# Optimization experiments

Hardware: AMD Instinct MI355X
Metric: run time of the kernel (lower is better)

## Reference

```python
import jax, jax.numpy as jnp
import numpy as np

NUM_LOOP = 10


def gru_cell(x, h, W_ih, W_hh, b_ih, b_hh):
    # torch.nn.GRUCell math. x, h: [N, H]; W_ih, W_hh: [3H, H]; b: [3H]
    gi = x @ W_ih.T + b_ih
    gh = h @ W_hh.T + b_hh
    i_r, i_z, i_n = jnp.split(gi, 3, axis=-1)
    h_r, h_z, h_n = jnp.split(gh, 3, axis=-1)
    r = jax.nn.sigmoid(i_r + h_r)
    z = jax.nn.sigmoid(i_z + h_z)
    n = jnp.tanh(i_n + r * h_n)
    return (1.0 - z) * n + z * h


def setup_inputs() -> dict:
    key = jax.random.key(0)
    ks = jax.random.split(key, 16)
    B, S, L, H, V = 16, 128, 128, 128, 50000
    input_var = jax.random.randint(ks[0], (B, S, L), 0, V, dtype=jnp.int32)
    adjacency = (jax.random.uniform(ks[1], (B, S, L, L)) < 0.05).astype(jnp.float32)
    u = lambda k, shp, a: jax.random.uniform(k, shp, minval=-a, maxval=a, dtype=jnp.float32)
    emb = jax.random.normal(ks[2], (V, H), dtype=jnp.float32) * 0.1
    gnn_w = u(ks[3], (H, H), 0.08)
    gnn_b = u(ks[4], (H,), 0.08)
    W_ih = u(ks[5], (3 * H, H), 0.08)
    W_hh = u(ks[6], (3 * H, H), 0.08)
    b_ih = u(ks[7], (3 * H,), 0.08)
    b_hh = u(ks[8], (3 * H,), 0.08)
    mW1 = u(ks[9], (H, H), 0.08)
    mb1 = u(ks[10], (H,), 0.08)
    mW2 = u(ks[11], (H, H), 0.08)
    mb2 = u(ks[12], (H,), 0.08)
    mW3 = u(ks[13], (1, H), 0.08)
    mb3 = u(ks[14], (1,), 0.08)
    return dict(input_var=input_var, adjacency=adjacency, emb=emb, gnn_w=gnn_w,
                gnn_b=gnn_b, W_ih=W_ih, W_hh=W_hh, b_ih=b_ih, b_hh=b_hh,
                mW1=mW1, mb1=mb1, mW2=mW2, mb2=mb2, mW3=mW3, mb3=mb3)


def reference(input_var, adjacency, emb, gnn_w, gnn_b, W_ih, W_hh, b_ih, b_hh,
              mW1, mb1, mW2, mb2, mW3, mb3):
    B, S, L = input_var.shape
    H = emb.shape[1]
    node_feature = emb[input_var]  # [B, S, L, H]

    def body(i, nf):
        tmp = nf @ gnn_w + gnn_b                      # [B,S,L,H] linear transform
        agg = jnp.matmul(adjacency, tmp)              # [B,S,L,L] @ [B,S,L,H]
        h = gru_cell(agg.reshape(-1, H), nf.reshape(-1, H), W_ih, W_hh, b_ih, b_hh)
        return h.reshape(B, S, L, H)

    node_feature = jax.lax.fori_loop(0, NUM_LOOP, body, node_feature)
    x = node_feature.reshape(B, S * L, H)
    # mention_predictor: 3-layer MLP with tanh after every layer (incl. last)
    h1 = jnp.tanh(x @ mW1.T + mb1)
    h2 = jnp.tanh(h1 @ mW2.T + mb2)
    mention_score = jnp.tanh(h2 @ mW3.T + mb3)        # [B, S*L, 1]
    return mention_score.reshape(B, S * L)
```

## Files before the change

kernel.cpp:

```cpp
#include <hip/hip_runtime.h>
#include <stdint.h>

typedef __bf16 bf16x8 __attribute__((ext_vector_type(8)));
typedef float  f32x4  __attribute__((ext_vector_type(4)));
typedef unsigned short ushortx4 __attribute__((ext_vector_type(4)));

#define LDS_NFROW 0
#define LDS_NFT   32768
#define LDS_P     65536
#define LDS_SAT   98304
#define LDS_RSA   131072
#define LDS_GB2   131584
#define LDS_BIH   133120
#define LDS_BHH   134656
#define LDS_MB1   136192
#define LDS_MB2   136704
#define LDS_TOTAL 137216

#define WS_GW2T   0
#define WS_WHH    98304
#define WS_MW1    196608
#define WS_MW2    229376
#define WS_GB2    262144

__device__ __forceinline__ unsigned short f2bf(float f){
  union{float f; uint32_t u;} v; v.f = f;
  return (unsigned short)((v.u + 0x7FFFu + ((v.u>>16)&1u)) >> 16);
}
__device__ __forceinline__ float bf2f(unsigned short h){
  union{uint32_t u; float f;} v; v.u = ((uint32_t)h)<<16; return v.f;
}
__device__ __forceinline__ float fast_sigmoid(float x){
  float t = __builtin_amdgcn_exp2f(-1.442695041f*x);
  return __builtin_amdgcn_rcpf(1.0f + t);
}
__device__ __forceinline__ float fast_tanh(float x){
  float t = __builtin_amdgcn_exp2f(-2.885390082f*x);
  return 2.0f*__builtin_amdgcn_rcpf(1.0f + t) - 1.0f;
}
__device__ __forceinline__ uint32_t sw(uint32_t row, uint32_t col){
  return row*256u + ((((col>>3) ^ (row&7)) << 4) | ((col&7)<<1));
}

extern "C" __global__ __launch_bounds__(128) void gnn_prep(
    const float* __restrict__ Wih, const float* __restrict__ Whh,
    const float* __restrict__ gnnw, const float* __restrict__ gnnb,
    const float* __restrict__ mW1, const float* __restrict__ mW2,
    unsigned short* __restrict__ gw2t, unsigned short* __restrict__ whhb,
    unsigned short* __restrict__ mw1b, unsigned short* __restrict__ mw2b,
    float* __restrict__ gb2)
{
  __shared__ float wg[128];
  const int b = blockIdx.x, t = threadIdx.x;
  if (b < 384){
    wg[t] = Wih[b*128 + t];
    __syncthreads();
    float acc = 0.f;
    for (int h=0; h<128; ++h) acc += wg[h] * gnnw[t*128 + h];
    gw2t[b*128 + t] = f2bf(acc);
    if (t == 0){
      float a2 = 0.f;
      for (int h=0; h<128; ++h) a2 += wg[h] * gnnb[h];
      gb2[b] = a2;
    }
  } else if (b < 416){
    int base = (b-384)*1536;
    for (int i=t; i<1536; i+=128) whhb[base+i] = f2bf(Whh[base+i]);
  } else if (b < 432){
    int base = (b-416)*1024;
    for (int i=t; i<1024; i+=128) mw1b[base+i] = f2bf(mW1[base+i]);
  } else if (b < 448){
    int base = (b-432)*1024;
    for (int i=t; i<1024; i+=128) mw2b[base+i] = f2bf(mW2[base+i]);
  }
}

extern "C" __global__ __launch_bounds__(512) void gnn_main(
    const int* __restrict__ iv, const float* __restrict__ adj,
    const float* __restrict__ emb,
    const float* __restrict__ bih, const float* __restrict__ bhh,
    const float* __restrict__ mb1, const float* __restrict__ mb2,
    const float* __restrict__ mW3, const float* __restrict__ mb3,
    const __bf16* __restrict__ gw2t, const __bf16* __restrict__ whhb,
    const __bf16* __restrict__ mw1b, const __bf16* __restrict__ mw2b,
    const float* __restrict__ gb2, float* __restrict__ out)
{
  extern __shared__ char lds[];
  const int bs   = blockIdx.x;
  const int tid  = threadIdx.x;
  const int w    = tid >> 6;
  const int lane = tid & 63;
  const int n16  = lane & 15;
  const int q    = lane >> 4;
  const f32x4 zf4 = {0.f, 0.f, 0.f, 0.f};

  if (tid < 384){
    *(float*)(lds + LDS_GB2 + tid*4) = gb2[tid];
    *(float*)(lds + LDS_BIH + tid*4) = bih[tid];
    *(float*)(lds + LDS_BHH + tid*4) = bhh[tid];
  }
  if (tid >= 384){
    int t = tid - 384;
    *(float*)(lds + LDS_MB1 + t*4) = mb1[t];
    *(float*)(lds + LDS_MB2 + t*4) = mb2[t];
  }

  {
    const int l  = tid >> 2;
    const int hc = (tid & 3) * 32;
    const int row = iv[bs*128 + l];
    const float* src = emb + (size_t)row*128 + hc;
    #pragma unroll
    for (int c=0; c<4; ++c){
      float4 f0 = *(const float4*)(src + c*8);
      float4 f1 = *(const float4*)(src + c*8 + 4);
      union{ bf16x8 v; unsigned short s8[8]; } u;
      u.s8[0]=f2bf(f0.x); u.s8[1]=f2bf(f0.y); u.s8[2]=f2bf(f0.z); u.s8[3]=f2bf(f0.w);
      u.s8[4]=f2bf(f1.x); u.s8[5]=f2bf(f1.y); u.s8[6]=f2bf(f1.z); u.s8[7]=f2bf(f1.w);
      *(bf16x8*)(lds + LDS_NFROW + sw(l, hc + c*8)) = u.v;
      #pragma unroll
      for (int j=0; j<8; ++j)
        *(unsigned short*)(lds + LDS_NFT + sw(hc + c*8 + j, l)) = u.s8[j];
    }
  }

  {
    const float* abase = adj + (size_t)bs * 16384;
    #pragma unroll
    for (int k=0; k<4; ++k){
      int s   = k*512 + tid;
      int sl  = s & 63;
      int chk = s >> 6;
      int ltg = chk >> 2, ks = chk & 3;
      int al  = ltg*16 + (sl & 15);
      int ak  = ks*32 + (sl >> 4) * 8;
      const float* p = abase + al*128 + ak;
      float4 f0 = *(const float4*)(p);
      float4 f1 = *(const float4*)(p + 4);
      union{ bf16x8 v; unsigned short s8[8]; } u;
      u.s8[0]=f2bf(f0.x); u.s8[1]=f2bf(f0.y); u.s8[2]=f2bf(f0.z); u.s8[3]=f2bf(f0.w);
      u.s8[4]=f2bf(f1.x); u.s8[5]=f2bf(f1.y); u.s8[6]=f2bf(f1.z); u.s8[7]=f2bf(f1.w);
      *(bf16x8*)(lds + LDS_SAT + s*16) = u.v;
    }
    int l = tid >> 2, p4 = tid & 3;
    const float* p = abase + l*128 + p4*32;
    float ssum = 0.f;
    #pragma unroll
    for (int c=0; c<8; ++c){
      float4 f = *(const float4*)(p + c*4);
      ssum += f.x + f.y + f.z + f.w;
    }
    ssum += __shfl_xor(ssum, 1);
    ssum += __shfl_xor(ssum, 2);
    if (p4 == 0) *(float*)(lds + LDS_RSA + l*4) = ssum;
  }
  __syncthreads();

  const int wr = w & 1, wc = w >> 1;
  const int t0 = wr*64, l0 = wc*32;
  const int h0 = w*16;

  const __bf16* gAr = gw2t + (size_t)(h0       + n16) * 128;
  const __bf16* gAz = gw2t + (size_t)(h0 + 128 + n16) * 128;
  const __bf16* gAn = gw2t + (size_t)(h0 + 256 + n16) * 128;
  const __bf16* hAr = whhb + (size_t)(h0       + n16) * 128;
  const __bf16* hAz = whhb + (size_t)(h0 + 128 + n16) * 128;
  const __bf16* hAn = whhb + (size_t)(h0 + 256 + n16) * 128;

  for (int it=0; it<10; ++it){
    f32x4 accA[4][2];
    #pragma unroll
    for (int a=0; a<4; ++a){ accA[a][0] = zf4; accA[a][1] = zf4; }
    for (int ks=0; ks<4; ++ks){
      bf16x8 af[4];
      #pragma unroll
      for (int tt=0; tt<4; ++tt)
        af[tt] = *(const bf16x8*)(lds + LDS_NFT + sw(t0 + tt*16 + n16, ks*32 + q*8));
      #pragma unroll
      for (int lb=0; lb<2; ++lb){
        int chunk = (wc*2 + lb)*4 + ks;
        bf16x8 bfb = *(const bf16x8*)(lds + LDS_SAT + (chunk*64 + lane)*16);
        #pragma unroll
        for (int tt=0; tt<4; ++tt)
          accA[tt][lb] = __builtin_amdgcn_mfma_f32_16x16x32_bf16(af[tt], bfb, accA[tt][lb], 0,0,0);
      }
    }
    #pragma unroll
    for (int tt=0; tt<4; ++tt){
      #pragma unroll
      for (int lb=0; lb<2; ++lb){
        int l  = l0 + lb*16 + n16;
        int tb = t0 + tt*16 + q*4;
        ushortx4 o4;
        #pragma unroll
        for (int r=0; r<4; ++r) o4[r] = f2bf(accA[tt][lb][r]);
        *(ushortx4*)(lds + LDS_P + sw(l, tb)) = o4;
      }
    }
    __syncthreads();

    f32x4 aR[8], aZ[8], aGN[8], aHN[8];
    #pragma unroll
    for (int i=0; i<8; ++i){ aR[i]=zf4; aZ[i]=zf4; aGN[i]=zf4; aHN[i]=zf4; }
    for (int ks=0; ks<4; ++ks){
      int koff = ks*32 + q*8;
      bf16x8 f_gr = *(const bf16x8*)(gAr + koff);
      bf16x8 f_gz = *(const bf16x8*)(gAz + koff);
      bf16x8 f_gn = *(const bf16x8*)(gAn + koff);
      bf16x8 f_hr = *(const bf16x8*)(hAr + koff);
      bf16x8 f_hz = *(const bf16x8*)(hAz + koff);
      bf16x8 f_hn = *(const bf16x8*)(hAn + koff);
      #pragma unroll
      for (int lt=0; lt<8; ++lt){
        int l = lt*16 + n16;
        bf16x8 bp = *(const bf16x8*)(lds + LDS_P     + sw(l, koff));
        bf16x8 bh = *(const bf16x8*)(lds + LDS_NFROW + sw(l, koff));
        aR[lt]  = __builtin_amdgcn_mfma_f32_16x16x32_bf16(f_gr, bp, aR[lt], 0,0,0);
        aR[lt]  = __builtin_amdgcn_mfma_f32_16x16x32_bf16(f_hr, bh, aR[lt], 0,0,0);
        aZ[lt]  = __builtin_amdgcn_mfma_f32_16x16x32_bf16(f_gz, bp, aZ[lt], 0,0,0);
        aZ[lt]  = __builtin_amdgcn_mfma_f32_16x16x32_bf16(f_hz, bh, aZ[lt], 0,0,0);
        aGN[lt] = __builtin_amdgcn_mfma_f32_16x16x32_bf16(f_gn, bp, aGN[lt], 0,0,0);
        aHN[lt] = __builtin_amdgcn_mfma_f32_16x16x32_bf16(f_hn, bh, aHN[lt], 0,0,0);
      }
    }
    __syncthreads();

    float c_gr[4], c_gz[4], c_gn[4], c_br[4], c_bz[4], c_bin[4], c_bhn[4];
    #pragma unroll
    for (int r=0; r<4; ++r){
      int h = h0 + q*4 + r;
      c_gr[r]  = *(const float*)(lds + LDS_GB2 + h*4);
      c_gz[r]  = *(const float*)(lds + LDS_GB2 + (128+h)*4);
      c_gn[r]  = *(const float*)(lds + LDS_GB2 + (256+h)*4);
      c_br[r]  = *(const float*)(lds + LDS_BIH + h*4)       + *(const float*)(lds + LDS_BHH + h*4);
      c_bz[r]  = *(const float*)(lds + LDS_BIH + (128+h)*4) + *(const float*)(lds + LDS_BHH + (128+h)*4);
      c_bin[r] = *(const float*)(lds + LDS_BIH + (256+h)*4);
      c_bhn[r] = *(const float*)(lds + LDS_BHH + (256+h)*4);
    }
    #pragma unroll
    for (int lt=0; lt<8; ++lt){
      int l = lt*16 + n16;
      float rs = *(const float*)(lds + LDS_RSA + l*4);
      uint32_t a_nf = sw(l, h0 + q*4);
      ushortx4 old4 = *(const ushortx4*)(lds + LDS_NFROW + a_nf);
      ushortx4 new4;
      #pragma unroll
      for (int r=0; r<4; ++r){
        float xr = aR[lt][r] + rs*c_gr[r] + c_br[r];
        float xz = aZ[lt][r] + rs*c_gz[r] + c_bz[r];
        float rg = fast_sigmoid(xr);
        float zg = fast_sigmoid(xz);
        float xn = (aGN[lt][r] + rs*c_gn[r] + c_bin[r]) + rg*(aHN[lt][r] + c_bhn[r]);
        float ng = fast_tanh(xn);
        float hv = bf2f(old4[r]);
        new4[r] = f2bf(ng + zg*(hv - ng));
      }
      *(ushortx4*)(lds + LDS_NFROW + a_nf) = new4;
      #pragma unroll
      for (int r=0; r<4; ++r)
        *(unsigned short*)(lds + LDS_NFT + sw(h0 + q*4 + r, l)) = new4[r];
    }
    __syncthreads();
  }

  {
    f32x4 acc[4][2];
    #pragma unroll
    for (int a=0; a<4; ++a){ acc[a][0] = zf4; acc[a][1] = zf4; }
    for (int ks=0; ks<4; ++ks){
      int koff = ks*32 + q*8;
      bf16x8 af[4];
      #pragma unroll
      for (int tt=0; tt<4; ++tt)
        af[tt] = *(const bf16x8*)(mw1b + (size_t)(t0 + tt*16 + n16)*128 + koff);
      #pragma unroll
      for (int lb=0; lb<2; ++lb){
        int l = l0 + lb*16 + n16;
        bf16x8 bb = *(const bf16x8*)(lds + LDS_NFROW + sw(l, koff));
        #pragma unroll
        for (int tt=0; tt<4; ++tt)
          acc[tt][lb] = __builtin_amdgcn_mfma_f32_16x16x32_bf16(af[tt], bb, acc[tt][lb], 0,0,0);
      }
    }
    #pragma unroll
    for (int tt=0; tt<4; ++tt){
      #pragma unroll
      for (int lb=0; lb<2; ++lb){
        int l  = l0 + lb*16 + n16;
        int ob = t0 + tt*16 + q*4;
        ushortx4 o4;
        #pragma unroll
        for (int r=0; r<4; ++r){
          float bsv = *(const float*)(lds + LDS_MB1 + (ob + r)*4);
          o4[r] = f2bf(fast_tanh(acc[tt][lb][r] + bsv));
        }
        *(ushortx4*)(lds + LDS_P + sw(l, ob)) = o4;
      }
    }
  }
  __syncthreads();

  {
    f32x4 acc[4][2];
    #pragma unroll
    for (int a=0; a<4; ++a){ acc[a][0] = zf4; acc[a][1] = zf4; }
    for (int ks=0; ks<4; ++ks){
      int koff = ks*32 + q*8;
      bf16x8 af[4];
      #pragma unroll
      for (int tt=0; tt<4; ++tt)
        af[tt] = *(const bf16x8*)(mw2b + (size_t)(t0 + tt*16 + n16)*128 + koff);
      #pragma unroll
      for (int lb=0; lb<2; ++lb){
        int l = l0 + lb*16 + n16;
        bf16x8 bb = *(const bf16x8*)(lds + LDS_P + sw(l, koff));
        #pragma unroll
        for (int tt=0; tt<4; ++tt)
          acc[tt][lb] = __builtin_amdgcn_mfma_f32_16x16x32_bf16(af[tt], bb, acc[tt][lb], 0,0,0);
      }
    }
    #pragma unroll
    for (int tt=0; tt<4; ++tt){
      #pragma unroll
      for (int lb=0; lb<2; ++lb){
        int l  = l0 + lb*16 + n16;
        int ob = t0 + tt*16 + q*4;
        ushortx4 o4;
        #pragma unroll
        for (int r=0; r<4; ++r){
          float bsv = *(const float*)(lds + LDS_MB2 + (ob + r)*4);
          o4[r] = f2bf(fast_tanh(acc[tt][lb][r] + bsv));
        }
        *(ushortx4*)(lds + LDS_NFT + sw(l, ob)) = o4;
      }
    }
  }
  __syncthreads();

  {
    int l = tid >> 2, p4 = tid & 3;
    float dot = 0.f;
    #pragma unroll
    for (int c=0; c<4; ++c){
      int o = p4*32 + c*8;
      union{ bf16x8 v; unsigned short s8[8]; } u;
      u.v = *(const bf16x8*)(lds + LDS_NFT + sw(l, o));
      float4 w0 = *(const float4*)(mW3 + o);
      float4 w1 = *(const float4*)(mW3 + o + 4);
      dot += bf2f(u.s8[0])*w0.x + bf2f(u.s8[1])*w0.y + bf2f(u.s8[2])*w0.z + bf2f(u.s8[3])*w0.w
           + bf2f(u.s8[4])*w1.x + bf2f(u.s8[5])*w1.y + bf2f(u.s8[6])*w1.z + bf2f(u.s8[7])*w1.w;
    }
    dot += __shfl_xor(dot, 1);
    dot += __shfl_xor(dot, 2);
    if (p4 == 0) out[bs*128 + l] = fast_tanh(dot + mb3[0]);
  }
}

extern "C" void kernel_launch(void* const* d_in, const int* in_sizes, int n_in,
                              void* d_out, int out_size, void* d_ws, size_t ws_size,
                              hipStream_t stream)
{
  const int*   iv   = (const int*)  d_in[0];
  const float* adj  = (const float*)d_in[1];
  const float* emb  = (const float*)d_in[2];
  const float* gnnw = (const float*)d_in[3];
  const float* gnnb = (const float*)d_in[4];
  const float* Wih  = (const float*)d_in[5];
  const float* Whh  = (const float*)d_in[6];
  const float* bihp = (const float*)d_in[7];
  const float* bhhp = (const float*)d_in[8];
  const float* mW1  = (const float*)d_in[9];
  const float* mb1  = (const float*)d_in[10];
  const float* mW2  = (const float*)d_in[11];
  const float* mb2  = (const float*)d_in[12];
  const float* mW3  = (const float*)d_in[13];
  const float* mb3  = (const float*)d_in[14];
  float* out = (float*)d_out;

  char* ws = (char*)d_ws;
  unsigned short* gw2t_w = (unsigned short*)(ws + WS_GW2T);
  unsigned short* whhb_w = (unsigned short*)(ws + WS_WHH);
  unsigned short* mw1b_w = (unsigned short*)(ws + WS_MW1);
  unsigned short* mw2b_w = (unsigned short*)(ws + WS_MW2);
  float*          gb2_w  = (float*)(ws + WS_GB2);

  hipFuncSetAttribute((const void*)gnn_main,
                      hipFuncAttributeMaxDynamicSharedMemorySize, LDS_TOTAL);

  gnn_prep<<<448, 128, 0, stream>>>(Wih, Whh, gnnw, gnnb, mW1, mW2,
                                    gw2t_w, whhb_w, mw1b_w, mw2b_w, gb2_w);

  int nbs = in_sizes[0] / 128;
  gnn_main<<<nbs, 512, LDS_TOTAL, stream>>>(
      iv, adj, emb, bihp, bhhp, mb1, mb2, mW3, mb3,
      (const __bf16*)gw2t_w, (const __bf16*)whhb_w,
      (const __bf16*)mw1b_w, (const __bf16*)mw2b_w, gb2_w, out);
}
```

Before: 2.245 ms.

## Double block size to 1024 threads and split per-wave GEMM tiles

Raises the workgroup from 8 to 16 waves per (batch, sentence) block, halving each wave's share of the adjacency GEMM, the fused GRU GEMMs, and the MLP GEMMs. Two waves now share each 16-row hidden slice, each taking half the node tiles. All loader and reduction loops are re-indexed for 1024 threads. The aim is more latency hiding within one CU, since LDS use (~134KB) allows only one block per CU. In exchange, more waves compete at each barrier, and the launch-bounds change constrains the register budget.

```diff
diff --git a/kernel.cpp b/kernel.cpp
--- a/kernel.cpp
+++ b/kernel.cpp
@@ -75,7 +75,7 @@
   }
 }
 
-extern "C" __global__ __launch_bounds__(512) void gnn_main(
+extern "C" __global__ __launch_bounds__(1024, 4) void gnn_main(
     const int* __restrict__ iv, const float* __restrict__ adj,
     const float* __restrict__ emb,
     const float* __restrict__ bih, const float* __restrict__ bhh,
@@ -98,20 +98,19 @@
     *(float*)(lds + LDS_GB2 + tid*4) = gb2[tid];
     *(float*)(lds + LDS_BIH + tid*4) = bih[tid];
     *(float*)(lds + LDS_BHH + tid*4) = bhh[tid];
-  }
-  if (tid >= 384){
+  } else if (tid < 512){
     int t = tid - 384;
     *(float*)(lds + LDS_MB1 + t*4) = mb1[t];
     *(float*)(lds + LDS_MB2 + t*4) = mb2[t];
   }
 
   {
-    const int l  = tid >> 2;
-    const int hc = (tid & 3) * 32;
+    const int l  = tid >> 3;
+    const int hc = (tid & 7) * 16;
     const int row = iv[bs*128 + l];
     const float* src = emb + (size_t)row*128 + hc;
     #pragma unroll
-    for (int c=0; c<4; ++c){
+    for (int c=0; c<2; ++c){
       float4 f0 = *(const float4*)(src + c*8);
       float4 f1 = *(const float4*)(src + c*8 + 4);
       union{ bf16x8 v; unsigned short s8[8]; } u;
@@ -127,8 +126,8 @@
   {
     const float* abase = adj + (size_t)bs * 16384;
     #pragma unroll
-    for (int k=0; k<4; ++k){
-      int s   = k*512 + tid;
+    for (int k=0; k<2; ++k){
+      int s   = k*1024 + tid;
       int sl  = s & 63;
       int chk = s >> 6;
       int ltg = chk >> 2, ks = chk & 3;
@@ -142,23 +141,27 @@
       u.s8[4]=f2bf(f1.x); u.s8[5]=f2bf(f1.y); u.s8[6]=f2bf(f1.z); u.s8[7]=f2bf(f1.w);
       *(bf16x8*)(lds + LDS_SAT + s*16) = u.v;
     }
-    int l = tid >> 2, p4 = tid & 3;
-    const float* p = abase + l*128 + p4*32;
+    int l = tid >> 3, p8 = tid & 7;
+    const float* p = abase + l*128 + p8*16;
     float ssum = 0.f;
     #pragma unroll
-    for (int c=0; c<8; ++c){
+    for (int c=0; c<4; ++c){
       float4 f = *(const float4*)(p + c*4);
       ssum += f.x + f.y + f.z + f.w;
     }
     ssum += __shfl_xor(ssum, 1);
     ssum += __shfl_xor(ssum, 2);
-    if (p4 == 0) *(float*)(lds + LDS_RSA + l*4) = ssum;
+    ssum += __shfl_xor(ssum, 4);
+    if (p8 == 0) *(float*)(lds + LDS_RSA + l*4) = ssum;
   }
   __syncthreads();
 
-  const int wr = w & 1, wc = w >> 1;
-  const int t0 = wr*64, l0 = wc*32;
-  const int h0 = w*16;
+  const int wr = w & 3, wc = w >> 2;
+  const int t0 = wr*32, l0 = wc*32;
+  const int wg   = w >> 1;
+  const int half = w & 1;
+  const int h0   = wg*16;
+  const int lt0  = half*4;
 
   const __bf16* gAr = gw2t + (size_t)(h0       + n16) * 128;
   const __bf16* gAz = gw2t + (size_t)(h0 + 128 + n16) * 128;
@@ -168,25 +171,25 @@
   const __bf16* hAn = whhb + (size_t)(h0 + 256 + n16) * 128;
 
   for (int it=0; it<10; ++it){
-    f32x4 accA[4][2];
-    #pragma unroll
-    for (int a=0; a<4; ++a){ accA[a][0] = zf4; accA[a][1] = zf4; }
+    f32x4 accA[2][2];
+    #pragma unroll
+    for (int a=0; a<2; ++a){ accA[a][0] = zf4; accA[a][1] = zf4; }
     for (int ks=0; ks<4; ++ks){
-      bf16x8 af[4];
-      #pragma unroll
-      for (int tt=0; tt<4; ++tt)
+      bf16x8 af[2];
+      #pragma unroll
+      for (int tt=0; tt<2; ++tt)
         af[tt] = *(const bf16x8*)(lds + LDS_NFT + sw(t0 + tt*16 + n16, ks*32 + q*8));
       #pragma unroll
       for (int lb=0; lb<2; ++lb){
         int chunk = (wc*2 + lb)*4 + ks;
         bf16x8 bfb = *(const bf16x8*)(lds + LDS_SAT + (chunk*64 + lane)*16);
         #pragma unroll
-        for (int tt=0; tt<4; ++tt)
+        for (int tt=0; tt<2; ++tt)
           accA[tt][lb] = __builtin_amdgcn_mfma_f32_16x16x32_bf16(af[tt], bfb, accA[tt][lb], 0,0,0);
       }
     }
     #pragma unroll
-    for (int tt=0; tt<4; ++tt){
+    for (int tt=0; tt<2; ++tt){
       #pragma unroll
       for (int lb=0; lb<2; ++lb){
         int l  = l0 + lb*16 + n16;
@@ -199,9 +202,9 @@
     }
     __syncthreads();
 
-    f32x4 aR[8], aZ[8], aGN[8], aHN[8];
-    #pragma unroll
-    for (int i=0; i<8; ++i){ aR[i]=zf4; aZ[i]=zf4; aGN[i]=zf4; aHN[i]=zf4; }
+    f32x4 aR[4], aZ[4], aGN[4], aHN[4];
+    #pragma unroll
+    for (int i=0; i<4; ++i){ aR[i]=zf4; aZ[i]=zf4; aGN[i]=zf4; aHN[i]=zf4; }
     for (int ks=0; ks<4; ++ks){
       int koff = ks*32 + q*8;
       bf16x8 f_gr = *(const bf16x8*)(gAr + koff);
@@ -211,16 +214,16 @@
       bf16x8 f_hz = *(const bf16x8*)(hAz + koff);
       bf16x8 f_hn = *(const bf16x8*)(hAn + koff);
       #pragma unroll
-      for (int lt=0; lt<8; ++lt){
-        int l = lt*16 + n16;
+      for (int i=0; i<4; ++i){
+        int l = (lt0 + i)*16 + n16;
         bf16x8 bp = *(const bf16x8*)(lds + LDS_P     + sw(l, koff));
         bf16x8 bh = *(const bf16x8*)(lds + LDS_NFROW + sw(l, koff));
-        aR[lt]  = __builtin_amdgcn_mfma_f32_16x16x32_bf16(f_gr, bp, aR[lt], 0,0,0);
-        aR[lt]  = __builtin_amdgcn_mfma_f32_16x16x32_bf16(f_hr, bh, aR[lt], 0,0,0);
-        aZ[lt]  = __builtin_amdgcn_mfma_f32_16x16x32_bf16(f_gz, bp, aZ[lt], 0,0,0);
-        aZ[lt]  = __builtin_amdgcn_mfma_f32_16x16x32_bf16(f_hz, bh, aZ[lt], 0,0,0);
-        aGN[lt] = __builtin_amdgcn_mfma_f32_16x16x32_bf16(f_gn, bp, aGN[lt], 0,0,0);
-        aHN[lt] = __builtin_amdgcn_mfma_f32_16x16x32_bf16(f_hn, bh, aHN[lt], 0,0,0);
+        aR[i]  = __builtin_amdgcn_mfma_f32_16x16x32_bf16(f_gr, bp, aR[i], 0,0,0);
+        aR[i]  = __builtin_amdgcn_mfma_f32_16x16x32_bf16(f_hr, bh, aR[i], 0,0,0);
+        aZ[i]  = __builtin_amdgcn_mfma_f32_16x16x32_bf16(f_gz, bp, aZ[i], 0,0,0);
+        aZ[i]  = __builtin_amdgcn_mfma_f32_16x16x32_bf16(f_hz, bh, aZ[i], 0,0,0);
+        aGN[i] = __builtin_amdgcn_mfma_f32_16x16x32_bf16(f_gn, bp, aGN[i], 0,0,0);
+        aHN[i] = __builtin_amdgcn_mfma_f32_16x16x32_bf16(f_hn, bh, aHN[i], 0,0,0);
       }
     }
     __syncthreads();
@@ -238,19 +241,19 @@
       c_bhn[r] = *(const float*)(lds + LDS_BHH + (256+h)*4);
     }
     #pragma unroll
-    for (int lt=0; lt<8; ++lt){
-      int l = lt*16 + n16;
+    for (int i=0; i<4; ++i){
+      int l = (lt0 + i)*16 + n16;
       float rs = *(const float*)(lds + LDS_RSA + l*4);
       uint32_t a_nf = sw(l, h0 + q*4);
       ushortx4 old4 = *(const ushortx4*)(lds + LDS_NFROW + a_nf);
       ushortx4 new4;
       #pragma unroll
       for (int r=0; r<4; ++r){
-        float xr = aR[lt][r] + rs*c_gr[r] + c_br[r];
-        float xz = aZ[lt][r] + rs*c_gz[r] + c_bz[r];
+        float xr = aR[i][r] + rs*c_gr[r] + c_br[r];
+        float xz = aZ[i][r] + rs*c_gz[r] + c_bz[r];
         float rg = fast_sigmoid(xr);
         float zg = fast_sigmoid(xz);
-        float xn = (aGN[lt][r] + rs*c_gn[r] + c_bin[r]) + rg*(aHN[lt][r] + c_bhn[r]);
+        float xn = (aGN[i][r] + rs*c_gn[r] + c_bin[r]) + rg*(aHN[i][r] + c_bhn[r]);
         float ng = fast_tanh(xn);
         float hv = bf2f(old4[r]);
         new4[r] = f2bf(ng + zg*(hv - ng));
@@ -264,26 +267,26 @@
   }
 
   {
-    f32x4 acc[4][2];
-    #pragma unroll
-    for (int a=0; a<4; ++a){ acc[a][0] = zf4; acc[a][1] = zf4; }
+    f32x4 acc[2][2];
+    #pragma unroll
+    for (int a=0; a<2; ++a){ acc[a][0] = zf4; acc[a][1] = zf4; }
     for (int ks=0; ks<4; ++ks){
       int koff = ks*32 + q*8;
-      bf16x8 af[4];
-      #pragma unroll
-      for (int tt=0; tt<4; ++tt)
+      bf16x8 af[2];
+      #pragma unroll
+      for (int tt=0; tt<2; ++tt)
         af[tt] = *(const bf16x8*)(mw1b + (size_t)(t0 + tt*16 + n16)*128 + koff);
       #pragma unroll
       for (int lb=0; lb<2; ++lb){
         int l = l0 + lb*16 + n16;
         bf16x8 bb = *(const bf16x8*)(lds + LDS_NFROW + sw(l, koff));
         #pragma unroll
-        for (int tt=0; tt<4; ++tt)
+        for (int tt=0; tt<2; ++tt)
           acc[tt][lb] = __builtin_amdgcn_mfma_f32_16x16x32_bf16(af[tt], bb, acc[tt][lb], 0,0,0);
       }
     }
     #pragma unroll
-    for (int tt=0; tt<4; ++tt){
+    for (int tt=0; tt<2; ++tt){
       #pragma unroll
       for (int lb=0; lb<2; ++lb){
         int l  = l0 + lb*16 + n16;
@@ -301,26 +304,26 @@
   __syncthreads();
 
   {
-    f32x4 acc[4][2];
-    #pragma unroll
-    for (int a=0; a<4; ++a){ acc[a][0] = zf4; acc[a][1] = zf4; }
+    f32x4 acc[2][2];
+    #pragma unroll
+    for (int a=0; a<2; ++a){ acc[a][0] = zf4; acc[a][1] = zf4; }
     for (int ks=0; ks<4; ++ks){
       int koff = ks*32 + q*8;
-      bf16x8 af[4];
-      #pragma unroll
-      for (int tt=0; tt<4; ++tt)
+      bf16x8 af[2];
+      #pragma unroll
+      for (int tt=0; tt<2; ++tt)
         af[tt] = *(const bf16x8*)(mw2b + (size_t)(t0 + tt*16 + n16)*128 + koff);
       #pragma unroll
       for (int lb=0; lb<2; ++lb){
         int l = l0 + lb*16 + n16;
         bf16x8 bb = *(const bf16x8*)(lds + LDS_P + sw(l, koff));
         #pragma unroll
-        for (int tt=0; tt<4; ++tt)
+        for (int tt=0; tt<2; ++tt)
           acc[tt][lb] = __builtin_amdgcn_mfma_f32_16x16x32_bf16(af[tt], bb, acc[tt][lb], 0,0,0);
       }
     }
     #pragma unroll
-    for (int tt=0; tt<4; ++tt){
+    for (int tt=0; tt<2; ++tt){
       #pragma unroll
       for (int lb=0; lb<2; ++lb){
         int l  = l0 + lb*16 + n16;
@@ -338,11 +341,11 @@
   __syncthreads();
 
   {
-    int l = tid >> 2, p4 = tid & 3;
+    int l = tid >> 3, p8 = tid & 7;
     float dot = 0.f;
     #pragma unroll
-    for (int c=0; c<4; ++c){
-      int o = p4*32 + c*8;
+    for (int c=0; c<2; ++c){
+      int o = p8*16 + c*8;
       union{ bf16x8 v; unsigned short s8[8]; } u;
       u.v = *(const bf16x8*)(lds + LDS_NFT + sw(l, o));
       float4 w0 = *(const float4*)(mW3 + o);
@@ -352,7 +355,8 @@
     }
     dot += __shfl_xor(dot, 1);
     dot += __shfl_xor(dot, 2);
-    if (p4 == 0) out[bs*128 + l] = fast_tanh(dot + mb3[0]);
+    dot += __shfl_xor(dot, 4);
+    if (p8 == 0) out[bs*128 + l] = fast_tanh(dot + mb3[0]);
   }
 }
 
@@ -391,7 +395,7 @@
                                     gw2t_w, whhb_w, mw1b_w, mw2b_w, gb2_w);
 
   int nbs = in_sizes[0] / 128;
-  gnn_main<<<nbs, 512, LDS_TOTAL, stream>>>(
+  gnn_main<<<nbs, 1024, LDS_TOTAL, stream>>>(
       iv, adj, emb, bihp, bhhp, mb1, mb2, mW3, mb3,
       (const __bf16*)gw2t_w, (const __bf16*)whhb_w,
       (const __bf16*)mw1b_w, (const __bf16*)mw2b_w, gb2_w, out);
```

New measurement: 2.528 ms. +12.6%, slower.
